# Performance work log

Measured on AMD Instinct MI355X. Metric: run time of the kernel, lower is better.

The kernel has to match this reference:

```python
import jax, jax.numpy as jnp
import numpy as np

B, S, D, H = 2, 2048, 1024, 16
DEPTH = D // H


def setup_inputs() -> dict:
    key = jax.random.key(0)
    ks = jax.random.split(key, 11)
    s = 1.0 / np.sqrt(D)
    inp = {
        "v": jax.random.normal(ks[0], (B, S, D), jnp.float32),
        "k": jax.random.normal(ks[1], (B, S, D), jnp.float32),
        "q": jax.random.normal(ks[2], (B, S, D), jnp.float32),
        # causal look-ahead mask: 1 where attention is disallowed
        "mask": (1.0 - jnp.tril(jnp.ones((S, S), jnp.float32)))[None, None, :, :],
        "Wq": jax.random.normal(ks[3], (D, D), jnp.float32) * s,
        "bq": jnp.zeros((D,), jnp.float32),
        "Wk": jax.random.normal(ks[4], (D, D), jnp.float32) * s,
        "bk": jnp.zeros((D,), jnp.float32),
        "Wv": jax.random.normal(ks[5], (D, D), jnp.float32) * s,
        "bv": jnp.zeros((D,), jnp.float32),
        "Wo": jax.random.normal(ks[6], (D, D), jnp.float32) * s,
        "bo": jnp.zeros((D,), jnp.float32),
    }
    return inp


def _split_heads(x):
    # (B, S, D) -> (B, H, S, depth)
    return x.reshape(B, -1, H, DEPTH).transpose(0, 2, 1, 3)


def reference(v, k, q, mask, Wq, bq, Wk, bk, Wv, bv, Wo, bo):
    qh = _split_heads(q @ Wq + bq)
    kh = _split_heads(k @ Wk + bk)
    vh = _split_heads(v @ Wv + bv)
    scale = 1.0 / jnp.sqrt(jnp.asarray(DEPTH, jnp.float32))
    logits = jnp.einsum("bhqd,bhkd->bhqk", qh, kh) * scale  # (B,H,S,S)
    logits = logits + mask * (-1e9)
    attn = jax.nn.softmax(logits, axis=-1)
    ctx = jnp.einsum("bhqk,bhkd->bhqd", attn, vh)
    concat = ctx.transpose(0, 2, 1, 3).reshape(B, -1, D)
    out = concat @ Wo + bo
    return out, attn
```

## Files before the change

kernel.cpp:

```cpp
#include <hip/hip_runtime.h>
#include <cstddef>
#include <cstdint>
#include <math.h>

#define Bsz   2
#define Sdim  2048
#define Hn    16
#define Ddim  1024
#define DEPTH 64
#define Mrows (Bsz * Sdim)
#define QTILES (Sdim / 64)

typedef __attribute__((ext_vector_type(8))) short short8v;
typedef __attribute__((ext_vector_type(4))) float f32x4;

__device__ __forceinline__ uint32_t pack_hl(float x) {
    const uint32_t u  = __float_as_uint(x);
    const uint32_t hi = u & 0xFFFF0000u;
    const float    r  = x - __uint_as_float(hi);
    const uint32_t v  = __float_as_uint(r);
    const uint32_t lo = (v + 0x7FFFu + ((v >> 16) & 1u)) >> 16;
    return hi | lo;
}

__device__ __forceinline__ void unpack_frag(const uint4& r0, const uint4& r1,
                                            short8v& hi, short8v& lo)
{
    union { uint32_t u[4]; short8v v; } H, L;
    const uint32_t p[8] = {r0.x, r0.y, r0.z, r0.w, r1.x, r1.y, r1.z, r1.w};
#pragma unroll
    for (int q = 0; q < 4; ++q) {
        const uint32_t p0 = p[2 * q], p1 = p[2 * q + 1];
        H.u[q] = (p0 >> 16) | (p1 & 0xFFFF0000u);
        L.u[q] = (p0 & 0xFFFFu) | (p1 << 16);
    }
    hi = H.v; lo = L.v;
}

__global__ __launch_bounds__(256) void pack_w_kernel(const float* __restrict__ W,
                                                     uint32_t* __restrict__ Wt)
{
    __shared__ uint32_t T[64][65];
    const int n0  = blockIdx.x * 64;
    const int k0  = blockIdx.y * 64;
    const int tid = threadIdx.x;
    const int c   = tid & 63;
    const int r0  = tid >> 6;
#pragma unroll
    for (int i = 0; i < 16; ++i) {
        const int kk = r0 * 16 + i;
        T[c][kk] = pack_hl(W[(size_t)(k0 + kk) * 1024 + n0 + c]);
    }
    __syncthreads();
#pragma unroll
    for (int i = 0; i < 16; ++i) {
        const int nn = r0 * 16 + i;
        Wt[(size_t)(n0 + nn) * 1024 + k0 + c] = T[nn][c];
    }
}

template <bool SPLIT, bool PACK>
__device__ __forceinline__ void mfma_gemm(const float* __restrict__ X,
                                          const uint32_t* __restrict__ Wt,
                                          const float* __restrict__ bias,
                                          void* __restrict__ Yv,
                                          float oscale)
{
    constexpr int K = 1024;
    __shared__ __align__(16) uint32_t Apk[128][36];

    const int tid  = threadIdx.x;
    const int lane = tid & 63;
    const int wid  = tid >> 6;
    const int wr   = wid >> 1;
    const int wc   = wid & 1;
    const int l15  = lane & 15;
    const int lg   = lane >> 4;

    const int m0 = blockIdx.y * 128;
    const int n0 = blockIdx.x * 128;

    const int sr = tid >> 3;
    const int sk = (tid & 7) * 4;

    const uint32_t* wp[4];
#pragma unroll
    for (int fj = 0; fj < 4; ++fj)
        wp[fj] = Wt + (size_t)(n0 + wc * 64 + fj * 16 + l15) * K + lg * 8;

    f32x4 acc[4][4] = {};

    for (int k0 = 0; k0 < K; k0 += 32) {
        uint4 braw[4][2];
#pragma unroll
        for (int fj = 0; fj < 4; ++fj) {
            braw[fj][0] = *reinterpret_cast<const uint4*>(wp[fj] + k0);
            braw[fj][1] = *reinterpret_cast<const uint4*>(wp[fj] + k0 + 4);
        }

        uint4 apk[4];
#pragma unroll
        for (int i = 0; i < 4; ++i) {
            const float4 xv = *reinterpret_cast<const float4*>(
                &X[(size_t)(m0 + sr + i * 32) * K + k0 + sk]);
            apk[i].x = pack_hl(xv.x);
            apk[i].y = pack_hl(xv.y);
            apk[i].z = pack_hl(xv.z);
            apk[i].w = pack_hl(xv.w);
        }

        __syncthreads();
#pragma unroll
        for (int i = 0; i < 4; ++i)
            *reinterpret_cast<uint4*>(&Apk[sr + i * 32][sk]) = apk[i];
        __syncthreads();

        short8v bhi[4], blo[4];
#pragma unroll
        for (int fj = 0; fj < 4; ++fj)
            unpack_frag(braw[fj][0], braw[fj][1], bhi[fj], blo[fj]);

#pragma unroll
        for (int fi = 0; fi < 4; ++fi) {
            const uint32_t* ap = &Apk[wr * 64 + fi * 16 + l15][lg * 8];
            const uint4 a0 = *reinterpret_cast<const uint4*>(ap);
            const uint4 a1 = *reinterpret_cast<const uint4*>(ap + 4);
            short8v ahi, alo;
            unpack_frag(a0, a1, ahi, alo);
#pragma unroll
            for (int fj = 0; fj < 4; ++fj) {
                acc[fi][fj] = __builtin_amdgcn_mfma_f32_16x16x32_bf16(
                    ahi, bhi[fj], acc[fi][fj], 0, 0, 0);
                acc[fi][fj] = __builtin_amdgcn_mfma_f32_16x16x32_bf16(
                    ahi, blo[fj], acc[fi][fj], 0, 0, 0);
                acc[fi][fj] = __builtin_amdgcn_mfma_f32_16x16x32_bf16(
                    alo, bhi[fj], acc[fi][fj], 0, 0, 0);
            }
        }
    }

#pragma unroll
    for (int fj = 0; fj < 4; ++fj) {
        const int col = n0 + wc * 64 + fj * 16 + l15;
        const float bv = bias[col];
#pragma unroll
        for (int fi = 0; fi < 4; ++fi) {
#pragma unroll
            for (int j = 0; j < 4; ++j) {
                const int row = m0 + wr * 64 + fi * 16 + lg * 4 + j;
                const float val = (acc[fi][fj][j] + bv) * oscale;
                size_t idx;
                if (SPLIT) {
                    const int bb = row >> 11;
                    const int ss = row & 2047;
                    const int hh = col >> 6;
                    const int dd = col & 63;
                    idx = (((size_t)bb * Hn + hh) * Sdim + ss) * DEPTH + dd;
                } else {
                    idx = (size_t)row * Ddim + col;
                }
                if (PACK) ((uint32_t*)Yv)[idx] = pack_hl(val);
                else      ((float*)Yv)[idx]    = val;
            }
        }
    }
}

__global__ __launch_bounds__(256) void proj_kernel(
    const float* __restrict__ q, const float* __restrict__ k,
    const float* __restrict__ v,
    const uint32_t* __restrict__ WtQ, const uint32_t* __restrict__ WtK,
    const uint32_t* __restrict__ WtV,
    const float* __restrict__ bq, const float* __restrict__ bk,
    const float* __restrict__ bv,
    uint32_t* __restrict__ qh, uint32_t* __restrict__ kh,
    uint32_t* __restrict__ vh)
{
    const float* X; const uint32_t* W; const float* bias; uint32_t* Y;
    float sc = 1.0f;
    switch (blockIdx.z) {
        case 0:  X = q; W = WtQ; bias = bq; Y = qh; sc = 0.125f; break;
        case 1:  X = k; W = WtK; bias = bk; Y = kh; break;
        default: X = v; W = WtV; bias = bv; Y = vh; break;
    }
    mfma_gemm<true, true>(X, W, bias, Y, sc);
}

__global__ __launch_bounds__(256) void oproj_kernel(
    const float* __restrict__ ctx, const uint32_t* __restrict__ WtO,
    const float* __restrict__ bo, float* __restrict__ out)
{
    mfma_gemm<false, false>(ctx, WtO, bo, out, 1.0f);
}

__device__ __forceinline__ void qk_tile(const uint32_t* __restrict__ kh_head,
                                        int k0, int l15, int lg,
                                        const short8v* qhi, const short8v* qlo,
                                        f32x4* sacc)
{
#pragma unroll
    for (int fc = 0; fc < 4; ++fc) {
        const uint32_t* p = kh_head + (size_t)(k0 + fc * 16 + l15) * DEPTH + lg * 8;
        const uint4 r00 = *reinterpret_cast<const uint4*>(p);
        const uint4 r01 = *reinterpret_cast<const uint4*>(p + 4);
        const uint4 r10 = *reinterpret_cast<const uint4*>(p + 32);
        const uint4 r11 = *reinterpret_cast<const uint4*>(p + 36);
        short8v khi, klo;
        unpack_frag(r00, r01, khi, klo);
        sacc[fc] = __builtin_amdgcn_mfma_f32_16x16x32_bf16(qhi[0], khi, sacc[fc], 0, 0, 0);
        sacc[fc] = __builtin_amdgcn_mfma_f32_16x16x32_bf16(qhi[0], klo, sacc[fc], 0, 0, 0);
        sacc[fc] = __builtin_amdgcn_mfma_f32_16x16x32_bf16(qlo[0], khi, sacc[fc], 0, 0, 0);
        unpack_frag(r10, r11, khi, klo);
        sacc[fc] = __builtin_amdgcn_mfma_f32_16x16x32_bf16(qhi[1], khi, sacc[fc], 0, 0, 0);
        sacc[fc] = __builtin_amdgcn_mfma_f32_16x16x32_bf16(qhi[1], klo, sacc[fc], 0, 0, 0);
        sacc[fc] = __builtin_amdgcn_mfma_f32_16x16x32_bf16(qlo[1], khi, sacc[fc], 0, 0, 0);
    }
}

__global__ __launch_bounds__(256) void attn_mfma_kernel(
    const uint32_t* __restrict__ qpk, const uint32_t* __restrict__ kpk,
    const uint32_t* __restrict__ vpk,
    float* __restrict__ attn, float* __restrict__ ctx)
{
    __shared__ __align__(16) uint32_t Vt[64][68];
    __shared__ __align__(16) uint32_t Ps[64][68];

    const int n   = blockIdx.x;
    const int xcd = n & 7;
    const int s   = n >> 3;
    const int c   = ((s >> 5) << 3) | xcd;
    const int qt  = 31 - (s & 31);
    const int b   = c >> 4;
    const int h   = c & 15;

    const int tid  = threadIdx.x;
    const int lane = tid & 63;
    const int wid  = tid >> 6;
    const int l15  = lane & 15;
    const int lg   = lane >> 4;

    const size_t head = ((size_t)(b * Hn + h)) * Sdim * DEPTH;
    const int q0 = qt * 64;

    const uint32_t* kh_head = kpk + head;
    const uint32_t* vh_head = vpk + head;

    short8v qhi[2], qlo[2];
    {
        const uint32_t* qp = qpk + head +
            (size_t)(q0 + wid * 16 + l15) * DEPTH + lg * 8;
#pragma unroll
        for (int kk = 0; kk < 2; ++kk) {
            const uint4 r0 = *reinterpret_cast<const uint4*>(qp + kk * 32);
            const uint4 r1 = *reinterpret_cast<const uint4*>(qp + kk * 32 + 4);
            unpack_frag(r0, r1, qhi[kk], qlo[kk]);
        }
    }

    float m_r[4], s_r[4];
#pragma unroll
    for (int j = 0; j < 4; ++j) { m_r[j] = -INFINITY; s_r[j] = 0.f; }

    for (int kt = 0; kt <= qt; ++kt) {
        const int k0 = kt * 64;
        f32x4 sacc[4] = {};
        qk_tile(kh_head, k0, l15, lg, qhi, qlo, sacc);

        const bool diag = (kt == qt);
#pragma unroll
        for (int j = 0; j < 4; ++j) {
            const int qg = q0 + wid * 16 + lg * 4 + j;
            float v0 = sacc[0][j], v1 = sacc[1][j], v2 = sacc[2][j], v3 = sacc[3][j];
            if (diag) {
                if (k0 +  0 + l15 > qg) v0 = -INFINITY;
                if (k0 + 16 + l15 > qg) v1 = -INFINITY;
                if (k0 + 32 + l15 > qg) v2 = -INFINITY;
                if (k0 + 48 + l15 > qg) v3 = -INFINITY;
            }
            float tmax = fmaxf(fmaxf(v0, v1), fmaxf(v2, v3));
            tmax = fmaxf(tmax, __shfl_xor(tmax, 1, 64));
            tmax = fmaxf(tmax, __shfl_xor(tmax, 2, 64));
            tmax = fmaxf(tmax, __shfl_xor(tmax, 4, 64));
            tmax = fmaxf(tmax, __shfl_xor(tmax, 8, 64));

            const float mnew = fmaxf(m_r[j], tmax);
            float ps = __expf(v0 - mnew) + __expf(v1 - mnew) +
                       __expf(v2 - mnew) + __expf(v3 - mnew);
            ps += __shfl_xor(ps, 1, 64);
            ps += __shfl_xor(ps, 2, 64);
            ps += __shfl_xor(ps, 4, 64);
            ps += __shfl_xor(ps, 8, 64);

            s_r[j] = s_r[j] * __expf(m_r[j] - mnew) + ps;
            m_r[j] = mnew;
        }
    }

    float inv_s[4];
#pragma unroll
    for (int j = 0; j < 4; ++j) inv_s[j] = 1.f / s_r[j];

    f32x4 cacc[4] = {};

    const int vr = tid >> 2;
    const int vq = tid & 3;

    for (int kt = 0; kt <= qt; ++kt) {
        const int k0 = kt * 64;

        uint4 vraw[4];
#pragma unroll
        for (int i = 0; i < 4; ++i)
            vraw[i] = *reinterpret_cast<const uint4*>(
                vh_head + (size_t)(k0 + vr) * DEPTH + (vq + 4 * i) * 4);

        f32x4 sacc[4] = {};
        qk_tile(kh_head, k0, l15, lg, qhi, qlo, sacc);

        const bool diag = (kt == qt);
        uint32_t ppk[4][4];
#pragma unroll
        for (int j = 0; j < 4; ++j) {
            const int qg = q0 + wid * 16 + lg * 4 + j;
            float* arow = attn + ((size_t)(b * Hn + h) * Sdim + qg) * Sdim;
#pragma unroll
            for (int fc = 0; fc < 4; ++fc) {
                const int col = k0 + fc * 16 + l15;
                float p = __expf(sacc[fc][j] - m_r[j]) * inv_s[j];
                if (diag && col > qg) p = 0.f;
                arow[col] = p;
                ppk[fc][j] = pack_hl(p);
            }
        }

        __syncthreads();

#pragma unroll
        for (int i = 0; i < 4; ++i) {
            const int c0 = (vq + 4 * i) * 4;
            Vt[c0 + 0][vr] = vraw[i].x;
            Vt[c0 + 1][vr] = vraw[i].y;
            Vt[c0 + 2][vr] = vraw[i].z;
            Vt[c0 + 3][vr] = vraw[i].w;
        }
#pragma unroll
        for (int j = 0; j < 4; ++j)
#pragma unroll
            for (int fc = 0; fc < 4; ++fc)
                Ps[wid * 16 + lg * 4 + j][fc * 16 + l15] = ppk[fc][j];

        __syncthreads();

#pragma unroll
        for (int kk = 0; kk < 2; ++kk) {
            const uint32_t* pap = &Ps[wid * 16 + l15][kk * 32 + lg * 8];
            const uint4 a0 = *reinterpret_cast<const uint4*>(pap);
            const uint4 a1 = *reinterpret_cast<const uint4*>(pap + 4);
            short8v phi, plo;
            unpack_frag(a0, a1, phi, plo);
#pragma unroll
            for (int fc = 0; fc < 4; ++fc) {
                const uint32_t* pbp = &Vt[fc * 16 + l15][kk * 32 + lg * 8];
                const uint4 b0 = *reinterpret_cast<const uint4*>(pbp);
                const uint4 b1 = *reinterpret_cast<const uint4*>(pbp + 4);
                short8v vhi, vlo;
                unpack_frag(b0, b1, vhi, vlo);
                cacc[fc] = __builtin_amdgcn_mfma_f32_16x16x32_bf16(phi, vhi, cacc[fc], 0, 0, 0);
                cacc[fc] = __builtin_amdgcn_mfma_f32_16x16x32_bf16(phi, vlo, cacc[fc], 0, 0, 0);
                cacc[fc] = __builtin_amdgcn_mfma_f32_16x16x32_bf16(plo, vhi, cacc[fc], 0, 0, 0);
            }
        }
    }

#pragma unroll
    for (int fc = 0; fc < 4; ++fc)
#pragma unroll
        for (int j = 0; j < 4; ++j) {
            const int qg = q0 + wid * 16 + lg * 4 + j;
            ctx[((size_t)b * Sdim + qg) * Ddim + h * DEPTH + fc * 16 + l15] =
                cacc[fc][j];
        }
}

extern "C" void kernel_launch(void* const* d_in, const int* in_sizes, int n_in,
                              void* d_out, int out_size, void* d_ws, size_t ws_size,
                              hipStream_t stream)
{
    (void)in_sizes; (void)n_in; (void)out_size; (void)ws_size;

    const float* v  = (const float*)d_in[0];
    const float* k  = (const float*)d_in[1];
    const float* q  = (const float*)d_in[2];
    const float* Wq = (const float*)d_in[4];
    const float* bq = (const float*)d_in[5];
    const float* Wk = (const float*)d_in[6];
    const float* bk = (const float*)d_in[7];
    const float* Wv = (const float*)d_in[8];
    const float* bv = (const float*)d_in[9];
    const float* Wo = (const float*)d_in[10];
    const float* bo = (const float*)d_in[11];

    float* out  = (float*)d_out;
    float* attn = out + (size_t)Bsz * Sdim * Ddim;

    const size_t sz = (size_t)Bsz * Sdim * Ddim;
    float* ws  = (float*)d_ws;
    uint32_t* qh = (uint32_t*)ws;
    uint32_t* kh = qh + sz;
    uint32_t* vh = kh + sz;
    float*   ctx = (float*)(vh + sz);

    uint32_t* WtQ = (uint32_t*)ctx;
    uint32_t* WtK = WtQ + 1024 * 1024;
    uint32_t* WtV = WtK + 1024 * 1024;
    uint32_t* WtO = qh;

    dim3 gpk(16, 16);
    pack_w_kernel<<<gpk, 256, 0, stream>>>(Wq, WtQ);
    pack_w_kernel<<<gpk, 256, 0, stream>>>(Wk, WtK);
    pack_w_kernel<<<gpk, 256, 0, stream>>>(Wv, WtV);

    dim3 gproj(Ddim / 128, Mrows / 128, 3);
    proj_kernel<<<gproj, 256, 0, stream>>>(q, k, v, WtQ, WtK, WtV,
                                           bq, bk, bv, qh, kh, vh);

    attn_mfma_kernel<<<dim3(QTILES * Hn * Bsz), 256, 0, stream>>>(
        qh, kh, vh, attn, ctx);

    pack_w_kernel<<<gpk, 256, 0, stream>>>(Wo, WtO);

    dim3 gout(Ddim / 128, Mrows / 128);
    oproj_kernel<<<gout, 256, 0, stream>>>(ctx, WtO, bo, out);
}
```

Before: 1.118 ms.

## Store bf16 hi/lo split planes separately instead of interleaved packed words

Replaces the interleaved 32-bit hi|lo packing with separate bf16 hi and lo planes for inputs, weights, Q/K/V, P, V^T and ctx. MFMA operands now load directly as short8 vectors, with no per-fragment unpack shuffles. Inputs are pre-split by a new pack_x_kernel, staged in the attn output buffer, and that buffer is then cleared with an added zero kernel before attention. The cost is extra launches and full passes over memory for packing and zeroing.

```diff
diff --git a/kernel.cpp b/kernel.cpp
--- a/kernel.cpp
+++ b/kernel.cpp
@@ -10,8 +10,10 @@
 #define DEPTH 64
 #define Mrows (Bsz * Sdim)
 #define QTILES (Sdim / 64)
+#define SZ    ((size_t)Bsz * Sdim * Ddim)
 
 typedef __attribute__((ext_vector_type(8))) short short8v;
+typedef __attribute__((ext_vector_type(4))) short short4v;
 typedef __attribute__((ext_vector_type(4))) float f32x4;
 
 __device__ __forceinline__ uint32_t pack_hl(float x) {
@@ -23,22 +25,24 @@
     return hi | lo;
 }
 
-__device__ __forceinline__ void unpack_frag(const uint4& r0, const uint4& r1,
-                                            short8v& hi, short8v& lo)
-{
-    union { uint32_t u[4]; short8v v; } H, L;
-    const uint32_t p[8] = {r0.x, r0.y, r0.z, r0.w, r1.x, r1.y, r1.z, r1.w};
-#pragma unroll
-    for (int q = 0; q < 4; ++q) {
-        const uint32_t p0 = p[2 * q], p1 = p[2 * q + 1];
-        H.u[q] = (p0 >> 16) | (p1 & 0xFFFF0000u);
-        L.u[q] = (p0 & 0xFFFFu) | (p1 << 16);
-    }
-    hi = H.v; lo = L.v;
-}
-
-__global__ __launch_bounds__(256) void pack_w_kernel(const float* __restrict__ W,
-                                                     uint32_t* __restrict__ Wt)
+__global__ __launch_bounds__(256) void pack_x_kernel(
+    const float* __restrict__ X, short* __restrict__ hi, short* __restrict__ lo)
+{
+    const size_t i4 = (size_t)blockIdx.x * 256 + threadIdx.x;
+    const float4 x = reinterpret_cast<const float4*>(X)[i4];
+    const uint32_t p0 = pack_hl(x.x), p1 = pack_hl(x.y),
+                   p2 = pack_hl(x.z), p3 = pack_hl(x.w);
+    short4v h, l;
+    h[0] = (short)(p0 >> 16); h[1] = (short)(p1 >> 16);
+    h[2] = (short)(p2 >> 16); h[3] = (short)(p3 >> 16);
+    l[0] = (short)(p0 & 0xFFFF); l[1] = (short)(p1 & 0xFFFF);
+    l[2] = (short)(p2 & 0xFFFF); l[3] = (short)(p3 & 0xFFFF);
+    reinterpret_cast<short4v*>(hi)[i4] = h;
+    reinterpret_cast<short4v*>(lo)[i4] = l;
+}
+
+__global__ __launch_bounds__(256) void pack_w_kernel(
+    const float* __restrict__ W, short* __restrict__ Whi, short* __restrict__ Wlo)
 {
     __shared__ uint32_t T[64][65];
     const int n0  = blockIdx.x * 64;
@@ -55,19 +59,29 @@
 #pragma unroll
     for (int i = 0; i < 16; ++i) {
         const int nn = r0 * 16 + i;
-        Wt[(size_t)(n0 + nn) * 1024 + k0 + c] = T[nn][c];
-    }
-}
-
-template <bool SPLIT, bool PACK>
-__device__ __forceinline__ void mfma_gemm(const float* __restrict__ X,
-                                          const uint32_t* __restrict__ Wt,
-                                          const float* __restrict__ bias,
-                                          void* __restrict__ Yv,
-                                          float oscale)
+        const uint32_t t = T[nn][c];
+        Whi[(size_t)(n0 + nn) * 1024 + k0 + c] = (short)(t >> 16);
+        Wlo[(size_t)(n0 + nn) * 1024 + k0 + c] = (short)(t & 0xFFFF);
+    }
+}
+
+__global__ __launch_bounds__(256) void zero_kernel(float4* __restrict__ p)
+{
+    const size_t i = (size_t)blockIdx.x * 256 + threadIdx.x;
+    p[i] = make_float4(0.f, 0.f, 0.f, 0.f);
+}
+
+template <bool SPLIT>
+__device__ __forceinline__ void gemm_planes(
+    const short* __restrict__ Xhi, const short* __restrict__ Xlo,
+    const short* __restrict__ Whi, const short* __restrict__ Wlo,
+    const float* __restrict__ bias,
+    float* __restrict__ Y, short* __restrict__ Yhi, short* __restrict__ Ylo,
+    float oscale)
 {
     constexpr int K = 1024;
-    __shared__ __align__(16) uint32_t Apk[128][36];
+    __shared__ __align__(16) short Ahi[128][40];
+    __shared__ __align__(16) short Alo[128][40];
 
     const int tid  = threadIdx.x;
     const int lane = tid & 63;
@@ -80,61 +94,54 @@
     const int m0 = blockIdx.y * 128;
     const int n0 = blockIdx.x * 128;
 
-    const int sr = tid >> 3;
-    const int sk = (tid & 7) * 4;
-
-    const uint32_t* wp[4];
-#pragma unroll
-    for (int fj = 0; fj < 4; ++fj)
-        wp[fj] = Wt + (size_t)(n0 + wc * 64 + fj * 16 + l15) * K + lg * 8;
+    const int sr = tid >> 1;
+    const int sc = (tid & 1) * 16;
+
+    const short* wph[4]; const short* wpl[4];
+#pragma unroll
+    for (int fj = 0; fj < 4; ++fj) {
+        const size_t row = (size_t)(n0 + wc * 64 + fj * 16 + l15) * K + lg * 8;
+        wph[fj] = Whi + row;
+        wpl[fj] = Wlo + row;
+    }
+
+    const size_t abase = (size_t)(m0 + sr) * K + sc;
 
     f32x4 acc[4][4] = {};
 
     for (int k0 = 0; k0 < K; k0 += 32) {
-        uint4 braw[4][2];
+        short8v bh[4], bl[4];
 #pragma unroll
         for (int fj = 0; fj < 4; ++fj) {
-            braw[fj][0] = *reinterpret_cast<const uint4*>(wp[fj] + k0);
-            braw[fj][1] = *reinterpret_cast<const uint4*>(wp[fj] + k0 + 4);
-        }
-
-        uint4 apk[4];
-#pragma unroll
-        for (int i = 0; i < 4; ++i) {
-            const float4 xv = *reinterpret_cast<const float4*>(
-                &X[(size_t)(m0 + sr + i * 32) * K + k0 + sk]);
-            apk[i].x = pack_hl(xv.x);
-            apk[i].y = pack_hl(xv.y);
-            apk[i].z = pack_hl(xv.z);
-            apk[i].w = pack_hl(xv.w);
-        }
+            bh[fj] = *reinterpret_cast<const short8v*>(wph[fj] + k0);
+            bl[fj] = *reinterpret_cast<const short8v*>(wpl[fj] + k0);
+        }
+
+        const short8v xh0 = *reinterpret_cast<const short8v*>(Xhi + abase + k0);
+        const short8v xh1 = *reinterpret_cast<const short8v*>(Xhi + abase + k0 + 8);
+        const short8v xl0 = *reinterpret_cast<const short8v*>(Xlo + abase + k0);
+        const short8v xl1 = *reinterpret_cast<const short8v*>(Xlo + abase + k0 + 8);
 
         __syncthreads();
-#pragma unroll
-        for (int i = 0; i < 4; ++i)
-            *reinterpret_cast<uint4*>(&Apk[sr + i * 32][sk]) = apk[i];
+        *reinterpret_cast<short8v*>(&Ahi[sr][sc])     = xh0;
+        *reinterpret_cast<short8v*>(&Ahi[sr][sc + 8]) = xh1;
+        *reinterpret_cast<short8v*>(&Alo[sr][sc])     = xl0;
+        *reinterpret_cast<short8v*>(&Alo[sr][sc + 8]) = xl1;
         __syncthreads();
 
-        short8v bhi[4], blo[4];
-#pragma unroll
-        for (int fj = 0; fj < 4; ++fj)
-            unpack_frag(braw[fj][0], braw[fj][1], bhi[fj], blo[fj]);
-
 #pragma unroll
         for (int fi = 0; fi < 4; ++fi) {
-            const uint32_t* ap = &Apk[wr * 64 + fi * 16 + l15][lg * 8];
-            const uint4 a0 = *reinterpret_cast<const uint4*>(ap);
-            const uint4 a1 = *reinterpret_cast<const uint4*>(ap + 4);
-            short8v ahi, alo;
-            unpack_frag(a0, a1, ahi, alo);
+            const int ar = wr * 64 + fi * 16 + l15;
+            const short8v ah = *reinterpret_cast<const short8v*>(&Ahi[ar][lg * 8]);
+            const short8v al = *reinterpret_cast<const short8v*>(&Alo[ar][lg * 8]);
 #pragma unroll
             for (int fj = 0; fj < 4; ++fj) {
                 acc[fi][fj] = __builtin_amdgcn_mfma_f32_16x16x32_bf16(
-                    ahi, bhi[fj], acc[fi][fj], 0, 0, 0);
+                    ah, bh[fj], acc[fi][fj], 0, 0, 0);
                 acc[fi][fj] = __builtin_amdgcn_mfma_f32_16x16x32_bf16(
-                    ahi, blo[fj], acc[fi][fj], 0, 0, 0);
+                    ah, bl[fj], acc[fi][fj], 0, 0, 0);
                 acc[fi][fj] = __builtin_amdgcn_mfma_f32_16x16x32_bf16(
-                    alo, bhi[fj], acc[fi][fj], 0, 0, 0);
+                    al, bh[fj], acc[fi][fj], 0, 0, 0);
             }
         }
     }
@@ -149,81 +156,85 @@
             for (int j = 0; j < 4; ++j) {
                 const int row = m0 + wr * 64 + fi * 16 + lg * 4 + j;
                 const float val = (acc[fi][fj][j] + bv) * oscale;
-                size_t idx;
                 if (SPLIT) {
                     const int bb = row >> 11;
                     const int ss = row & 2047;
                     const int hh = col >> 6;
                     const int dd = col & 63;
-                    idx = (((size_t)bb * Hn + hh) * Sdim + ss) * DEPTH + dd;
+                    const size_t idx =
+                        (((size_t)bb * Hn + hh) * Sdim + ss) * DEPTH + dd;
+                    const uint32_t p = pack_hl(val);
+                    Yhi[idx] = (short)(p >> 16);
+                    Ylo[idx] = (short)(p & 0xFFFF);
                 } else {
-                    idx = (size_t)row * Ddim + col;
+                    Y[(size_t)row * Ddim + col] = val;
                 }
-                if (PACK) ((uint32_t*)Yv)[idx] = pack_hl(val);
-                else      ((float*)Yv)[idx]    = val;
             }
         }
     }
 }
 
 __global__ __launch_bounds__(256) void proj_kernel(
-    const float* __restrict__ q, const float* __restrict__ k,
-    const float* __restrict__ v,
-    const uint32_t* __restrict__ WtQ, const uint32_t* __restrict__ WtK,
-    const uint32_t* __restrict__ WtV,
+    const short* __restrict__ XqH, const short* __restrict__ XqL,
+    const short* __restrict__ XkH, const short* __restrict__ XkL,
+    const short* __restrict__ XvH, const short* __restrict__ XvL,
+    const short* __restrict__ WqH, const short* __restrict__ WqL,
+    const short* __restrict__ WkH, const short* __restrict__ WkL,
+    const short* __restrict__ WvH, const short* __restrict__ WvL,
     const float* __restrict__ bq, const float* __restrict__ bk,
     const float* __restrict__ bv,
-    uint32_t* __restrict__ qh, uint32_t* __restrict__ kh,
-    uint32_t* __restrict__ vh)
-{
-    const float* X; const uint32_t* W; const float* bias; uint32_t* Y;
+    short* __restrict__ qhH, short* __restrict__ qhL,
+    short* __restrict__ khH, short* __restrict__ khL,
+    short* __restrict__ vhH, short* __restrict__ vhL)
+{
+    const short *Xh, *Xl, *Wh, *Wl; const float* bias; short *Yh, *Yl;
     float sc = 1.0f;
     switch (blockIdx.z) {
-        case 0:  X = q; W = WtQ; bias = bq; Y = qh; sc = 0.125f; break;
-        case 1:  X = k; W = WtK; bias = bk; Y = kh; break;
-        default: X = v; W = WtV; bias = bv; Y = vh; break;
-    }
-    mfma_gemm<true, true>(X, W, bias, Y, sc);
+        case 0:  Xh=XqH; Xl=XqL; Wh=WqH; Wl=WqL; bias=bq; Yh=qhH; Yl=qhL; sc=0.125f; break;
+        case 1:  Xh=XkH; Xl=XkL; Wh=WkH; Wl=WkL; bias=bk; Yh=khH; Yl=khL; break;
+        default: Xh=XvH; Xl=XvL; Wh=WvH; Wl=WvL; bias=bv; Yh=vhH; Yl=vhL; break;
+    }
+    gemm_planes<true>(Xh, Xl, Wh, Wl, bias, nullptr, Yh, Yl, sc);
 }
 
 __global__ __launch_bounds__(256) void oproj_kernel(
-    const float* __restrict__ ctx, const uint32_t* __restrict__ WtO,
+    const short* __restrict__ ctxH, const short* __restrict__ ctxL,
+    const short* __restrict__ WoH, const short* __restrict__ WoL,
     const float* __restrict__ bo, float* __restrict__ out)
 {
-    mfma_gemm<false, false>(ctx, WtO, bo, out, 1.0f);
-}
-
-__device__ __forceinline__ void qk_tile(const uint32_t* __restrict__ kh_head,
-                                        int k0, int l15, int lg,
-                                        const short8v* qhi, const short8v* qlo,
-                                        f32x4* sacc)
+    gemm_planes<false>(ctxH, ctxL, WoH, WoL, bo, out, nullptr, nullptr, 1.0f);
+}
+
+__device__ __forceinline__ void qk_tile_pl(const short* __restrict__ kH,
+                                           const short* __restrict__ kL,
+                                           int k0, int l15, int lg,
+                                           const short8v* qhi, const short8v* qlo,
+                                           f32x4* sacc)
 {
 #pragma unroll
     for (int fc = 0; fc < 4; ++fc) {
-        const uint32_t* p = kh_head + (size_t)(k0 + fc * 16 + l15) * DEPTH + lg * 8;
-        const uint4 r00 = *reinterpret_cast<const uint4*>(p);
-        const uint4 r01 = *reinterpret_cast<const uint4*>(p + 4);
-        const uint4 r10 = *reinterpret_cast<const uint4*>(p + 32);
-        const uint4 r11 = *reinterpret_cast<const uint4*>(p + 36);
-        short8v khi, klo;
-        unpack_frag(r00, r01, khi, klo);
-        sacc[fc] = __builtin_amdgcn_mfma_f32_16x16x32_bf16(qhi[0], khi, sacc[fc], 0, 0, 0);
-        sacc[fc] = __builtin_amdgcn_mfma_f32_16x16x32_bf16(qhi[0], klo, sacc[fc], 0, 0, 0);
-        sacc[fc] = __builtin_amdgcn_mfma_f32_16x16x32_bf16(qlo[0], khi, sacc[fc], 0, 0, 0);
-        unpack_frag(r10, r11, khi, klo);
-        sacc[fc] = __builtin_amdgcn_mfma_f32_16x16x32_bf16(qhi[1], khi, sacc[fc], 0, 0, 0);
-        sacc[fc] = __builtin_amdgcn_mfma_f32_16x16x32_bf16(qhi[1], klo, sacc[fc], 0, 0, 0);
-        sacc[fc] = __builtin_amdgcn_mfma_f32_16x16x32_bf16(qlo[1], khi, sacc[fc], 0, 0, 0);
+        const size_t ro = (size_t)(k0 + fc * 16 + l15) * DEPTH + lg * 8;
+#pragma unroll
+        for (int kk = 0; kk < 2; ++kk) {
+            const short8v khi = *reinterpret_cast<const short8v*>(kH + ro + kk * 32);
+            const short8v klo = *reinterpret_cast<const short8v*>(kL + ro + kk * 32);
+            sacc[fc] = __builtin_amdgcn_mfma_f32_16x16x32_bf16(qhi[kk], khi, sacc[fc], 0, 0, 0);
+            sacc[fc] = __builtin_amdgcn_mfma_f32_16x16x32_bf16(qhi[kk], klo, sacc[fc], 0, 0, 0);
+            sacc[fc] = __builtin_amdgcn_mfma_f32_16x16x32_bf16(qlo[kk], khi, sacc[fc], 0, 0, 0);
+        }
     }
 }
 
 __global__ __launch_bounds__(256) void attn_mfma_kernel(
-    const uint32_t* __restrict__ qpk, const uint32_t* __restrict__ kpk,
-    const uint32_t* __restrict__ vpk,
-    float* __restrict__ attn, float* __restrict__ ctx)
-{
-    __shared__ __align__(16) uint32_t Vt[64][68];
-    __shared__ __align__(16) uint32_t Ps[64][68];
+    const short* __restrict__ qH, const short* __restrict__ qL,
+    const short* __restrict__ kH, const short* __restrict__ kL,
+    const short* __restrict__ vH, const short* __restrict__ vL,
+    float* __restrict__ attn, short* __restrict__ ctxH, short* __restrict__ ctxL)
+{
+    __shared__ __align__(16) short Vth[64][72];
+    __shared__ __align__(16) short Vtl[64][72];
+    __shared__ __align__(16) short Psh[64][72];
+    __shared__ __align__(16) short Psl[64][72];
 
     const int n   = blockIdx.x;
     const int xcd = n & 7;
@@ -242,18 +253,18 @@
     const size_t head = ((size_t)(b * Hn + h)) * Sdim * DEPTH;
     const int q0 = qt * 64;
 
-    const uint32_t* kh_head = kpk + head;
-    const uint32_t* vh_head = vpk + head;
+    const short* khh = kH + head;
+    const short* khl = kL + head;
+    const short* vhh = vH + head;
+    const short* vhl = vL + head;
 
     short8v qhi[2], qlo[2];
     {
-        const uint32_t* qp = qpk + head +
-            (size_t)(q0 + wid * 16 + l15) * DEPTH + lg * 8;
+        const size_t qo = head + (size_t)(q0 + wid * 16 + l15) * DEPTH + lg * 8;
 #pragma unroll
         for (int kk = 0; kk < 2; ++kk) {
-            const uint4 r0 = *reinterpret_cast<const uint4*>(qp + kk * 32);
-            const uint4 r1 = *reinterpret_cast<const uint4*>(qp + kk * 32 + 4);
-            unpack_frag(r0, r1, qhi[kk], qlo[kk]);
+            qhi[kk] = *reinterpret_cast<const short8v*>(qH + qo + kk * 32);
+            qlo[kk] = *reinterpret_cast<const short8v*>(qL + qo + kk * 32);
         }
     }
 
@@ -264,7 +275,7 @@
     for (int kt = 0; kt <= qt; ++kt) {
         const int k0 = kt * 64;
         f32x4 sacc[4] = {};
-        qk_tile(kh_head, k0, l15, lg, qhi, qlo, sacc);
+        qk_tile_pl(khh, khl, k0, l15, lg, qhi, qlo, sacc);
 
         const bool diag = (kt == qt);
 #pragma unroll
@@ -308,14 +319,14 @@
     for (int kt = 0; kt <= qt; ++kt) {
         const int k0 = kt * 64;
 
-        uint4 vraw[4];
-#pragma unroll
-        for (int i = 0; i < 4; ++i)
-            vraw[i] = *reinterpret_cast<const uint4*>(
-                vh_head + (size_t)(k0 + vr) * DEPTH + (vq + 4 * i) * 4);
+        const size_t vo = (size_t)(k0 + vr) * DEPTH + vq * 16;
+        const short8v vh0 = *reinterpret_cast<const short8v*>(vhh + vo);
+        const short8v vh1 = *reinterpret_cast<const short8v*>(vhh + vo + 8);
+        const short8v vl0 = *reinterpret_cast<const short8v*>(vhl + vo);
+        const short8v vl1 = *reinterpret_cast<const short8v*>(vhl + vo + 8);
 
         f32x4 sacc[4] = {};
-        qk_tile(kh_head, k0, l15, lg, qhi, qlo, sacc);
+        qk_tile_pl(khh, khl, k0, l15, lg, qhi, qlo, sacc);
 
         const bool diag = (kt == qt);
         uint32_t ppk[4][4];
@@ -336,38 +347,37 @@
         __syncthreads();
 
 #pragma unroll
-        for (int i = 0; i < 4; ++i) {
-            const int c0 = (vq + 4 * i) * 4;
-            Vt[c0 + 0][vr] = vraw[i].x;
-            Vt[c0 + 1][vr] = vraw[i].y;
-            Vt[c0 + 2][vr] = vraw[i].z;
-            Vt[c0 + 3][vr] = vraw[i].w;
+        for (int t = 0; t < 8; ++t) {
+            Vth[vq * 16 + t][vr]     = vh0[t];
+            Vth[vq * 16 + 8 + t][vr] = vh1[t];
+            Vtl[vq * 16 + t][vr]     = vl0[t];
+            Vtl[vq * 16 + 8 + t][vr] = vl1[t];
         }
 #pragma unroll
         for (int j = 0; j < 4; ++j)
 #pragma unroll
-            for (int fc = 0; fc < 4; ++fc)
-                Ps[wid * 16 + lg * 4 + j][fc * 16 + l15] = ppk[fc][j];
-
+            for (int fc = 0; fc < 4; ++fc) {
+                const uint32_t p = ppk[fc][j];
+                Psh[wid * 16 + lg * 4 + j][fc * 16 + l15] = (short)(p >> 16);
+                Psl[wid * 16 + lg * 4 + j][fc * 16 + l15] = (short)(p & 0xFFFF);
+            }
         __syncthreads();
 
 #pragma unroll
         for (int kk = 0; kk < 2; ++kk) {
-            const uint32_t* pap = &Ps[wid * 16 + l15][kk * 32 + lg * 8];
-            const uint4 a0 = *reinterpret_cast<const uint4*>(pap);
-            const uint4 a1 = *reinterpret_cast<const uint4*>(pap + 4);
-            short8v phi, plo;
-            unpack_frag(a0, a1, phi, plo);
+            const short8v ph = *reinterpret_cast<const short8v*>(
+                &Psh[wid * 16 + l15][kk * 32 + lg * 8]);
+            const short8v pl = *reinterpret_cast<const short8v*>(
+                &Psl[wid * 16 + l15][kk * 32 + lg * 8]);
 #pragma unroll
             for (int fc = 0; fc < 4; ++fc) {
-                const uint32_t* pbp = &Vt[fc * 16 + l15][kk * 32 + lg * 8];
-                const uint4 b0 = *reinterpret_cast<const uint4*>(pbp);
-                const uint4 b1 = *reinterpret_cast<const uint4*>(pbp + 4);
-                short8v vhi, vlo;
-                unpack_frag(b0, b1, vhi, vlo);
-                cacc[fc] = __builtin_amdgcn_mfma_f32_16x16x32_bf16(phi, vhi, cacc[fc], 0, 0, 0);
-                cacc[fc] = __builtin_amdgcn_mfma_f32_16x16x32_bf16(phi, vlo, cacc[fc], 0, 0, 0);
-                cacc[fc] = __builtin_amdgcn_mfma_f32_16x16x32_bf16(plo, vhi, cacc[fc], 0, 0, 0);
+                const short8v vh = *reinterpret_cast<const short8v*>(
+                    &Vth[fc * 16 + l15][kk * 32 + lg * 8]);
+                const short8v vl = *reinterpret_cast<const short8v*>(
+                    &Vtl[fc * 16 + l15][kk * 32 + lg * 8]);
+                cacc[fc] = __builtin_amdgcn_mfma_f32_16x16x32_bf16(ph, vh, cacc[fc], 0, 0, 0);
+                cacc[fc] = __builtin_amdgcn_mfma_f32_16x16x32_bf16(ph, vl, cacc[fc], 0, 0, 0);
+                cacc[fc] = __builtin_amdgcn_mfma_f32_16x16x32_bf16(pl, vh, cacc[fc], 0, 0, 0);
             }
         }
     }
@@ -377,8 +387,11 @@
 #pragma unroll
         for (int j = 0; j < 4; ++j) {
             const int qg = q0 + wid * 16 + lg * 4 + j;
-            ctx[((size_t)b * Sdim + qg) * Ddim + h * DEPTH + fc * 16 + l15] =
-                cacc[fc][j];
+            const size_t idx =
+                ((size_t)b * Sdim + qg) * Ddim + h * DEPTH + fc * 16 + l15;
+            const uint32_t p = pack_hl(cacc[fc][j]);
+            ctxH[idx] = (short)(p >> 16);
+            ctxL[idx] = (short)(p & 0xFFFF);
         }
 }
 
@@ -401,34 +414,44 @@
     const float* bo = (const float*)d_in[11];
 
     float* out  = (float*)d_out;
-    float* attn = out + (size_t)Bsz * Sdim * Ddim;
-
-    const size_t sz = (size_t)Bsz * Sdim * Ddim;
-    float* ws  = (float*)d_ws;
-    uint32_t* qh = (uint32_t*)ws;
-    uint32_t* kh = qh + sz;
-    uint32_t* vh = kh + sz;
-    float*   ctx = (float*)(vh + sz);
-
-    uint32_t* WtQ = (uint32_t*)ctx;
-    uint32_t* WtK = WtQ + 1024 * 1024;
-    uint32_t* WtV = WtK + 1024 * 1024;
-    uint32_t* WtO = qh;
+    float* attn = out + SZ;
+
+    short* w = (short*)d_ws;
+    short* qhH = w;            short* qhL = qhH + SZ;
+    short* khH = qhL + SZ;     short* khL = khH + SZ;
+    short* vhH = khL + SZ;     short* vhL = vhH + SZ;
+    short* ctxH = vhL + SZ;    short* ctxL = ctxH + SZ;
+    short* WoH = ctxL + SZ;    short* WoL = WoH + 1024 * 1024;
+
+    short* sc = (short*)attn;
+    short* XqH = sc;           short* XqL = XqH + SZ;
+    short* XkH = XqL + SZ;     short* XkL = XkH + SZ;
+    short* XvH = XkL + SZ;     short* XvL = XvH + SZ;
+    short* WqH = XvL + SZ;     short* WqL = WqH + 1024 * 1024;
+    short* WkH = WqL + 1024 * 1024;  short* WkL = WkH + 1024 * 1024;
+    short* WvH = WkL + 1024 * 1024;  short* WvL = WvH + 1024 * 1024;
 
     dim3 gpk(16, 16);
-    pack_w_kernel<<<gpk, 256, 0, stream>>>(Wq, WtQ);
-    pack_w_kernel<<<gpk, 256, 0, stream>>>(Wk, WtK);
-    pack_w_kernel<<<gpk, 256, 0, stream>>>(Wv, WtV);
+    pack_w_kernel<<<gpk, 256, 0, stream>>>(Wq, WqH, WqL);
+    pack_w_kernel<<<gpk, 256, 0, stream>>>(Wk, WkH, WkL);
+    pack_w_kernel<<<gpk, 256, 0, stream>>>(Wv, WvH, WvL);
+    pack_w_kernel<<<gpk, 256, 0, stream>>>(Wo, WoH, WoL);
+
+    pack_x_kernel<<<4096, 256, 0, stream>>>(q, XqH, XqL);
+    pack_x_kernel<<<4096, 256, 0, stream>>>(k, XkH, XkL);
+    pack_x_kernel<<<4096, 256, 0, stream>>>(v, XvH, XvL);
 
     dim3 gproj(Ddim / 128, Mrows / 128, 3);
-    proj_kernel<<<gproj, 256, 0, stream>>>(q, k, v, WtQ, WtK, WtV,
-                                           bq, bk, bv, qh, kh, vh);
+    proj_kernel<<<gproj, 256, 0, stream>>>(XqH, XqL, XkH, XkL, XvH, XvL,
+                                           WqH, WqL, WkH, WkL, WvH, WvL,
+                                           bq, bk, bv,
+                                           qhH, qhL, khH, khL, vhH, vhL);
+
+    zero_kernel<<<15360, 256, 0, stream>>>((float4*)attn);
 
     attn_mfma_kernel<<<dim3(QTILES * Hn * Bsz), 256, 0, stream>>>(
-        qh, kh, vh, attn, ctx);
-
-    pack_w_kernel<<<gpk, 256, 0, stream>>>(Wo, WtO);
+        qhH, qhL, khH, khL, vhH, vhL, attn, ctxH, ctxL);
 
     dim3 gout(Ddim / 128, Mrows / 128);
-    oproj_kernel<<<gout, 256, 0, stream>>>(ctx, WtO, bo, out);
-}
+    oproj_kernel<<<gout, 256, 0, stream>>>(ctxH, ctxL, WoH, WoL, bo, out);
+}
```

Result: slower. 1.162 ms (+3.9%).
